# Kernel optimization log

Hardware: AMD Instinct MI355X
Metric: run time of the kernel (lower is better)

## Reference

```python
import jax, jax.numpy as jnp
import numpy as np

B, T, H, NH = 4, 2048, 1024, 16
HD = H // NH  # 64


def setup_inputs() -> dict:
    key = jax.random.key(0)
    ks = jax.random.split(key, 8)
    s = 1.0 / np.sqrt(H)
    return {
        "hidden_states": jax.random.normal(ks[0], (B, T, H), dtype=jnp.float32),
        "attention_mask": jnp.zeros((B, 1, 1, T), dtype=jnp.float32),
        "Wq": jax.random.normal(ks[1], (H, H), dtype=jnp.float32) * s,
        "bq": jax.random.normal(ks[2], (H,), dtype=jnp.float32) * 0.01,
        "Wk": jax.random.normal(ks[3], (H, H), dtype=jnp.float32) * s,
        "bk": jax.random.normal(ks[4], (H,), dtype=jnp.float32) * 0.01,
        "Wv": jax.random.normal(ks[5], (H, H), dtype=jnp.float32) * s,
        "bv": jax.random.normal(ks[6], (H,), dtype=jnp.float32) * 0.01,
    }


def _split_heads(x):
    # [b, t, h*d] -> [b, h, t, d]
    b, t, _ = x.shape
    return x.reshape(b, t, NH, HD).transpose(0, 2, 1, 3)


def reference(hidden_states, attention_mask, Wq, bq, Wk, bk, Wv, bv):
    q = _split_heads(hidden_states @ Wq.T + bq)
    k = _split_heads(hidden_states @ Wk.T + bk)
    v = _split_heads(hidden_states @ Wv.T + bv)
    scores = jnp.einsum('bhqd,bhkd->bhqk', q, k) / jnp.sqrt(jnp.float32(HD))
    t = q.shape[2]
    causal = jnp.triu(jnp.ones((t, t), dtype=scores.dtype), k=1)[None, None] * (-1e9)
    scores = scores + causal + attention_mask
    probs = jax.nn.softmax(scores, axis=-1)
    # module returns [b, h, t, d] (no merge back)
    return jnp.einsum('bhqk,bhkd->bhqd', probs, v)
```

## Files before the change

kernel.cpp:

```cpp
#include <hip/hip_runtime.h>
#include <hip/hip_bf16.h>


typedef float  f32x4 __attribute__((ext_vector_type(4)));
typedef short  s16x8 __attribute__((ext_vector_type(8)));
typedef unsigned short u16;

#define LOG2E 1.44269504088896340736f

__device__ __forceinline__ u16 f2bf(float f) {
  unsigned u = __float_as_uint(f);
  u += 0x7FFFu + ((u >> 16) & 1u);
  return (u16)(u >> 16);
}
__device__ __forceinline__ float bf2f(u16 v) {
  return __uint_as_float(((unsigned)v) << 16);
}
__device__ __forceinline__ float ex2(float x) {
#if __has_builtin(__builtin_amdgcn_exp2f)
  return __builtin_amdgcn_exp2f(x);
#else
  return exp2f(x);
#endif
}
__device__ __forceinline__ float rcp_(float x) {
#if __has_builtin(__builtin_amdgcn_rcpf)
  return __builtin_amdgcn_rcpf(x);
#else
  return 1.0f / x;
#endif
}
__device__ __forceinline__ unsigned cvtpk(float lo, float hi) {
  unsigned r;
  asm("v_cvt_pk_bf16_f32 %0, %1, %2" : "=v"(r) : "v"(lo), "v"(hi));
  return r;
}
__device__ __forceinline__ void bar() {
  asm volatile("" ::: "memory");
  __builtin_amdgcn_s_barrier();
  asm volatile("" ::: "memory");
}

#define GLOAD16(gp, lp)                                                          \
  __builtin_amdgcn_global_load_lds(                                              \
      (const __attribute__((address_space(1))) void*)(gp),                       \
      (__attribute__((address_space(3))) void*)(lp), 16, 0, 0)

#define MFMA(a, b, c) __builtin_amdgcn_mfma_f32_16x16x32_bf16((a), (b), (c), 0, 0, 0)

__global__ __launch_bounds__(256) void cvt_all(
    const float* __restrict__ hs, const float* __restrict__ wq,
    const float* __restrict__ wk, const float* __restrict__ wv,
    const float* __restrict__ maskp,
    u16* __restrict__ xo, u16* __restrict__ qo, u16* __restrict__ ko,
    u16* __restrict__ vo, u16* __restrict__ wm) {
  int b = blockIdx.x;
  const float* s;
  u16* d;
  size_t i;
  bool isw = false;
  if (b < 4096) { s = hs; d = xo; i = (size_t)b * 256 + threadIdx.x; }
  else if (b < 5632) {
    int w = (b - 4096) >> 9, r = (b - 4096) & 511;
    s = (w == 0) ? wq : (w == 1) ? wk : wv;
    d = (w == 0) ? qo : (w == 1) ? ko : vo;
    i = (size_t)r * 256 + threadIdx.x;
  } else {
    s = maskp; d = wm; i = (size_t)(b - 5632) * 256 + threadIdx.x;
    isw = true;
  }
  const float4* sp = (const float4*)s + i * 2;
  float4 a = sp[0], c = sp[1];
  s16x8 r8;
  if (isw) {
    r8[0] = f2bf(ex2(a.x * LOG2E)); r8[1] = f2bf(ex2(a.y * LOG2E));
    r8[2] = f2bf(ex2(a.z * LOG2E)); r8[3] = f2bf(ex2(a.w * LOG2E));
    r8[4] = f2bf(ex2(c.x * LOG2E)); r8[5] = f2bf(ex2(c.y * LOG2E));
    r8[6] = f2bf(ex2(c.z * LOG2E)); r8[7] = f2bf(ex2(c.w * LOG2E));
  } else {
    r8[0] = f2bf(a.x); r8[1] = f2bf(a.y); r8[2] = f2bf(a.z); r8[3] = f2bf(a.w);
    r8[4] = f2bf(c.x); r8[5] = f2bf(c.y); r8[6] = f2bf(c.z); r8[7] = f2bf(c.w);
  }
  *(s16x8*)(d + i * 8) = r8;
}

__global__ __launch_bounds__(512, 2) void qkv_gemm(
    const u16* __restrict__ Xb,
    const u16* __restrict__ Wqb, const u16* __restrict__ Wkb,
    const u16* __restrict__ Wvb,
    const float* __restrict__ bq, const float* __restrict__ bk,
    const float* __restrict__ bv, const u16* __restrict__ Wm,
    u16* __restrict__ Qo, u16* __restrict__ Ko, u16* __restrict__ Vto) {
  int bid0 = blockIdx.x;
  int bid  = (bid0 & 7) * 48 + (bid0 >> 3);
  int which = bid % 3;
  int rt = bid / 3;
  int mt = rt >> 2, nt = rt & 3;
  const u16* W = (which == 0) ? Wqb : (which == 1) ? Wkb : Wvb;
  const float* bias = (which == 0) ? bq : (which == 1) ? bk : bv;

  __shared__ __align__(16) char lds[131072];

  int tid = threadIdx.x;
  int lane = tid & 63, wid = tid >> 6;
  int q16 = lane & 15, g = lane >> 4;
  int wr = wid >> 2, wc = wid & 3;

  int rloc = tid >> 3;
  int sw = ((tid & 7) ^ (rloc & 7)) << 4;
  const char* Asrc = (const char*)Xb + (size_t)(mt * 256 + rloc) * 2048 + sw;
  const char* Bsrc = (const char*)W  + (size_t)(nt * 256 + rloc) * 2048 + sw;

  int slot0 = (g ^ (q16 & 7)) << 4;

#define SA(u, h) do { size_t so = (size_t)(u) * 128 + (size_t)(h) * 262144;      \
    char* dd = lds + ((u) & 1) * 32768 + (h) * 16384 + tid * 16;                 \
    GLOAD16(Asrc + so, dd);                                                      \
    GLOAD16(Asrc + so + 131072, dd + 8192); } while (0)
#define SB(u, h) do { size_t so = (size_t)(u) * 128 + (size_t)(h) * 262144;      \
    char* dd = lds + 65536 + ((u) & 1) * 32768 + (h) * 16384 + tid * 16;         \
    GLOAD16(Bsrc + so, dd);                                                      \
    GLOAD16(Bsrc + so + 131072, dd + 8192); } while (0)

#define LDA8(kh, buf) do {                                                       \
    const char* p_ = lds + (buf) * 32768 + (wr * 128 + q16) * 128 +              \
                     (slot0 ^ ((kh) * 64));                                      \
    _Pragma("unroll")                                                            \
    for (int m_ = 0; m_ < 8; ++m_) fA[m_] = *(const s16x8*)(p_ + m_ * 2048); } while (0)

#define LDB2(nh, kh, buf) do {                                                   \
    const char* p_ = lds + 65536 + (buf) * 32768 +                               \
                     (wc * 64 + (nh) * 32 + q16) * 128 + (slot0 ^ ((kh) * 64));  \
    fB[0] = *(const s16x8*)(p_);                                                 \
    fB[1] = *(const s16x8*)(p_ + 2048); } while (0)

#define MM(nh) do {                                                              \
    __builtin_amdgcn_s_setprio(1);                                               \
    _Pragma("unroll")                                                            \
    for (int m_ = 0; m_ < 8; ++m_) {                                             \
      acc[m_][2 * (nh)]     = MFMA(fA[m_], fB[0], acc[m_][2 * (nh)]);            \
      acc[m_][2 * (nh) + 1] = MFMA(fA[m_], fB[1], acc[m_][2 * (nh) + 1]);        \
    }                                                                            \
    __builtin_amdgcn_s_setprio(0); } while (0)

  SA(0, 0); SA(0, 1); SB(0, 0); SB(0, 1);
  SA(1, 0);
  asm volatile("s_waitcnt vmcnt(2)" ::: "memory");
  bar();

  f32x4 acc[8][4] = {};
  s16x8 fA[8], fB[2];

#pragma unroll 1
  for (int t = 0; t < 16; ++t) {
    int buf = t & 1;
    LDA8(0, buf); LDB2(0, 0, buf);
    if (t < 15) SA(t + 1, 1);
    bar(); MM(0); bar();
    LDB2(1, 0, buf);
    if (t < 15) SB(t + 1, 0);
    bar(); MM(1); bar();
    LDA8(1, buf); LDB2(0, 1, buf);
    if (t < 15) SB(t + 1, 1);
    bar(); MM(0); bar();
    LDB2(1, 1, buf);
    if (t < 14) {
      SA(t + 2, 0);
      asm volatile("s_waitcnt vmcnt(2)" ::: "memory");
    } else if (t == 14) {
      asm volatile("s_waitcnt vmcnt(0)" ::: "memory");
    }
    bar(); MM(1); bar();
  }

  float qsc = (which == 0) ? (0.125f * LOG2E) : 1.0f;
  u16* Out = (which == 0) ? Qo : (which == 1) ? Ko : Vto;
  int h0 = nt * 4 + wc;
  u16* tile = (u16*)(void*)lds + (size_t)wid * 4608;
  const char* tb = (const char*)tile;
  int rl = lane >> 3, cb = (lane & 7) * 16;

#define EPIPASS(P) do {                                                          \
    int mbase = mt * 256 + wr * 128 + (P) * 64;                                  \
    int bb = mbase >> 11, t0 = mbase & 2047;                                     \
    if (which != 2) {                                                            \
      _Pragma("unroll")                                                          \
      for (int n = 0; n < 4; ++n) {                                              \
        float bvl = bias[h0 * 64 + n * 16 + q16];                                \
        _Pragma("unroll")                                                        \
        for (int mm = 0; mm < 4; ++mm)                                           \
          _Pragma("unroll")                                                      \
          for (int j = 0; j < 4; ++j)                                            \
            tile[(mm * 16 + g * 4 + j) * 72 + n * 16 + q16] =                    \
                f2bf((acc[(P) * 4 + mm][n][j] + bvl) * qsc);                     \
      }                                                                          \
    } else {                                                                     \
      const u16* wrow = Wm + (size_t)bb * 2048 + t0;                             \
      float wv[4][4];                                                            \
      _Pragma("unroll")                                                          \
      for (int mm = 0; mm < 4; ++mm)                                             \
        _Pragma("unroll")                                                        \
        for (int j = 0; j < 4; ++j)                                              \
          wv[mm][j] = bf2f(wrow[mm * 16 + g * 4 + j]);                           \
      _Pragma("unroll")                                                          \
      for (int n = 0; n < 4; ++n) {                                              \
        float bvl = bias[h0 * 64 + n * 16 + q16];                                \
        _Pragma("unroll")                                                        \
        for (int mm = 0; mm < 4; ++mm)                                           \
          _Pragma("unroll")                                                      \
          for (int j = 0; j < 4; ++j)                                            \
            tile[(n * 16 + q16) * 72 + mm * 16 + g * 4 + j] =                    \
                f2bf((acc[(P) * 4 + mm][n][j] + bvl) * wv[mm][j]);               \
      }                                                                          \
    }                                                                            \
    asm volatile("" ::: "memory");                                               \
    if (which != 2) {                                                            \
      char* gbase = (char*)(Out + ((size_t)(bb * 16 + h0) * 2048 + t0) * 64);    \
      _Pragma("unroll")                                                          \
      for (int c = 0; c < 8; ++c) {                                              \
        int row = rl + c * 8;                                                    \
        s16x8 v = *(const s16x8*)(tb + row * 144 + cb);                          \
        *(s16x8*)(gbase + row * 128 + cb) = v;                                   \
      }                                                                          \
    } else {                                                                     \
      char* gbase = (char*)Out + ((size_t)(bb * 16 + h0) * 64) * 4096 + t0 * 2;  \
      _Pragma("unroll")                                                          \
      for (int c = 0; c < 8; ++c) {                                              \
        int d = rl + c * 8;                                                      \
        s16x8 v = *(const s16x8*)(tb + d * 144 + cb);                            \
        *(s16x8*)(gbase + (size_t)d * 4096 + cb) = v;                            \
      }                                                                          \
    }                                                                            \
    asm volatile("" ::: "memory"); } while (0)

  EPIPASS(0);
  EPIPASS(1);
#undef EPIPASS
#undef SA
#undef SB
#undef LDA8
#undef LDB2
#undef MM
}

__global__ __launch_bounds__(256, 2) void attn_fwd(
    const u16* __restrict__ Qw, const u16* __restrict__ Kw,
    const u16* __restrict__ Vtw, const u16* __restrict__ Wm,
    float* __restrict__ out) {
  int bid0 = blockIdx.x;
  int bid = (bid0 & 7) * 64 + (bid0 >> 3);
  int bh = bid >> 3, p = bid & 7;
  int tid = threadIdx.x;
  int lane = tid & 63, wid = tid >> 6;
  int q16 = lane & 15, g = lane >> 4;

  __shared__ __align__(16) char Ks[3][8192];
  __shared__ __align__(16) char Vs[3][8192];
  __shared__ __align__(16) u16 wl[2048];

  int srow = tid >> 3;
  int sinner = (tid & 7) << 4;
  int fs = (srow & 7) ^ ((srow >> 1) & 4);
  int ssw = sinner ^ (fs << 4);
  const char* Kg = (const char*)Kw + ((size_t)bh * 2048 + srow) * 128 + ssw;
  const char* Vg = (const char*)Vtw + ((size_t)bh * 64 + srow) * 4096 + ssw;

#define STAGE_T(kt, b) do {                                                      \
    GLOAD16(Kg + (size_t)(kt) * 8192,        Ks[b] + tid * 16);                  \
    GLOAD16(Kg + (size_t)(kt) * 8192 + 4096, Ks[b] + tid * 16 + 4096);           \
    GLOAD16(Vg + (size_t)(kt) * 128,          Vs[b] + tid * 16);                 \
    GLOAD16(Vg + (size_t)(kt) * 128 + 131072, Vs[b] + tid * 16 + 4096); } while (0)

  GLOAD16((const char*)Wm + (size_t)(bh >> 4) * 4096 + tid * 16,
          (char*)wl + tid * 16);

  auto run_phase = [&](int qtl) {
    int nt = 2 * qtl + 2;
    int qw0 = (qtl << 7) + wid * 32;
    size_t qr = (size_t)bh * 2048 + qw0 + q16;
    s16x8 qa[2][2];
#pragma unroll
    for (int h = 0; h < 2; ++h) {
      qa[h][0] = *(const s16x8*)(Qw + (qr + 16 * h) * 64 + g * 8);
      qa[h][1] = *(const s16x8*)(Qw + (qr + 16 * h) * 64 + 32 + g * 8);
    }
    STAGE_T(0, 0);
    STAGE_T(1, 1);

    f32x4 o[2][4] = {};
    f32x4 lw[2] = {};
    int bc = 0;

#pragma unroll 1
    for (int kt = 0; kt < nt; ++kt) {
      if (kt + 2 < nt) {
        int bp = bc + 2; if (bp >= 3) bp -= 3;
        STAGE_T(kt + 2, bp);
        asm volatile("s_waitcnt vmcnt(8)" ::: "memory");
      } else if (kt + 1 < nt) {
        asm volatile("s_waitcnt vmcnt(4)" ::: "memory");
      } else {
        asm volatile("s_waitcnt vmcnt(0)" ::: "memory");
      }
      __builtin_amdgcn_s_barrier();
      asm volatile("" ::: "memory");

      if (64 * kt <= qw0 + 31) {
        int kb = kt << 6;
        const char* ksb = Ks[bc];
        const char* vsb = Vs[bc];
        bool causal = (64 * kt + 63 > qw0);
#pragma unroll
        for (int c = 0; c < 2; ++c) {
          f32x4 sA[2][2];
          __builtin_amdgcn_s_setprio(1);
#pragma unroll
          for (int t4 = 0; t4 < 2; ++t4) {
            int kk = 32 * c + ((q16 >> 2) << 3) + (t4 << 2) + (q16 & 3);
            int fk = (kk & 7) ^ ((kk >> 1) & 4);
            const char* krow = ksb + kk * 128;
            int in0 = (g * 16) ^ (fk << 4);
            s16x8 kf0 = *(const s16x8*)(krow + in0);
            s16x8 kf1 = *(const s16x8*)(krow + (in0 ^ 64));
#pragma unroll
            for (int h = 0; h < 2; ++h) {
              f32x4 sv = {0.f, 0.f, 0.f, 0.f};
              sv = MFMA(kf0, qa[h][0], sv);
              sv = MFMA(kf1, qa[h][1], sv);
              sA[t4][h] = sv;
            }
          }
          __builtin_amdgcn_s_setprio(0);

          s16x8 wf = *(const s16x8*)((const char*)wl + (kb + 32 * c + 8 * g) * 2);

          union { s16x8 v; unsigned u[4]; } pb[2];
#pragma unroll
          for (int h = 0; h < 2; ++h) {
            int qc = qw0 + 16 * h + q16;
#pragma unroll
            for (int t4 = 0; t4 < 2; ++t4) {
              float a0 = ex2(sA[t4][h][0]), a1 = ex2(sA[t4][h][1]);
              float a2 = ex2(sA[t4][h][2]), a3 = ex2(sA[t4][h][3]);
              if (causal) {
                int k0 = kb + 32 * c + 8 * g + 4 * t4;
                a0 = (k0 + 0 <= qc) ? a0 : 0.f;
                a1 = (k0 + 1 <= qc) ? a1 : 0.f;
                a2 = (k0 + 2 <= qc) ? a2 : 0.f;
                a3 = (k0 + 3 <= qc) ? a3 : 0.f;
              }
              pb[h].u[t4 * 2 + 0] = cvtpk(a0, a1);
              pb[h].u[t4 * 2 + 1] = cvtpk(a2, a3);
            }
          }

          __builtin_amdgcn_s_setprio(1);
#pragma unroll
          for (int dt = 0; dt < 4; ++dt) {
            int d = dt * 16 + q16;
            int fv = (d & 7) ^ ((d >> 1) & 4);
            s16x8 vf = *(const s16x8*)(vsb + d * 128 + ((64 * c + 16 * g) ^ (fv << 4)));
#pragma unroll
            for (int h = 0; h < 2; ++h)
              o[h][dt] = MFMA(vf, pb[h].v, o[h][dt]);
          }
#pragma unroll
          for (int h = 0; h < 2; ++h)
            lw[h] = MFMA(wf, pb[h].v, lw[h]);
          __builtin_amdgcn_s_setprio(0);
        }
      }
      __builtin_amdgcn_s_barrier();
      asm volatile("" ::: "memory");
      if (++bc >= 3) bc -= 3;
    }

#pragma unroll
    for (int h = 0; h < 2; ++h) {
      float inv = rcp_(lw[h][0]);
      float* op = out + ((size_t)bh * 2048 + qw0 + 16 * h + q16) * 64 + g * 4;
#pragma unroll
      for (int dt = 0; dt < 4; ++dt)
        *(f32x4*)(op + dt * 16) = o[h][dt] * inv;
    }
  };

  run_phase(15 - p);
  run_phase(p);
#undef STAGE_T
}

extern "C" void kernel_launch(void* const* d_in, const int* in_sizes, int n_in,
                              void* d_out, int out_size, void* d_ws, size_t ws_size,
                              hipStream_t stream) {
  const float* hs   = (const float*)d_in[0];
  const float* mask = (const float*)d_in[1];
  const float* Wq   = (const float*)d_in[2];
  const float* bq   = (const float*)d_in[3];
  const float* Wk   = (const float*)d_in[4];
  const float* bk   = (const float*)d_in[5];
  const float* Wv   = (const float*)d_in[6];
  const float* bv   = (const float*)d_in[7];
  float* out = (float*)d_out;

  char* w = (char*)d_ws;
  u16* Xb  = (u16*)w; w += (size_t)8192 * 1024 * 2;
  u16* Wqb = (u16*)w; w += (size_t)1024 * 1024 * 2;
  u16* Wkb = (u16*)w; w += (size_t)1024 * 1024 * 2;
  u16* Wvb = (u16*)w; w += (size_t)1024 * 1024 * 2;
  u16* Qw  = (u16*)w; w += (size_t)8192 * 1024 * 2;
  u16* Kw  = (u16*)w; w += (size_t)8192 * 1024 * 2;
  u16* Vtw = (u16*)w; w += (size_t)8192 * 1024 * 2;
  u16* Wm  = (u16*)w; w += (size_t)8192 * 2;

  cvt_all<<<5636, 256, 0, stream>>>(hs, Wq, Wk, Wv, mask, Xb, Wqb, Wkb, Wvb, Wm);
  qkv_gemm<<<384, 512, 0, stream>>>(Xb, Wqb, Wkb, Wvb, bq, bk, bv, Wm, Qw, Kw, Vtw);
  attn_fwd<<<512, 256, 0, stream>>>(Qw, Kw, Vtw, Wm, out);
}
```

Baseline: 135.7 us.

## Shrink QKV GEMM tiles to 128x128 with simple double-buffered K loop

Replaces the 256x256, 512-thread QKV projection GEMM that used a 128 KB LDS split-phase pipeline with a 128x128, 256-thread tile that double-buffers 32-wide K slices in 32 KB of LDS. The grid grows from 384 to 1536 blocks with three blocks per CU targeted, trading per-block operand reuse for more parallelism and occupancy across the 256 CUs. The epilogue is reworked for the smaller tile, and the mask weights for V are loaded once outside the passes. The risks are lower arithmetic intensity, more global and LDS traffic per FLOP, and a barrier on every short K step.

After: 136.8 us. Within noise of the previous version (+0.8%).

```diff
diff --git a/kernel.cpp b/kernel.cpp
--- a/kernel.cpp
+++ b/kernel.cpp
@@ -84,7 +84,7 @@
   *(s16x8*)(d + i * 8) = r8;
 }
 
-__global__ __launch_bounds__(512, 2) void qkv_gemm(
+__global__ __launch_bounds__(256, 3) void qkv_gemm(
     const u16* __restrict__ Xb,
     const u16* __restrict__ Wqb, const u16* __restrict__ Wkb,
     const u16* __restrict__ Wvb,
@@ -92,143 +92,126 @@
     const float* __restrict__ bv, const u16* __restrict__ Wm,
     u16* __restrict__ Qo, u16* __restrict__ Ko, u16* __restrict__ Vto) {
   int bid0 = blockIdx.x;
-  int bid  = (bid0 & 7) * 48 + (bid0 >> 3);
+  int bid  = (bid0 & 7) * 192 + (bid0 >> 3);
   int which = bid % 3;
   int rt = bid / 3;
-  int mt = rt >> 2, nt = rt & 3;
+  int mt = rt >> 3, ntl = rt & 7;
   const u16* W = (which == 0) ? Wqb : (which == 1) ? Wkb : Wvb;
   const float* bias = (which == 0) ? bq : (which == 1) ? bk : bv;
 
-  __shared__ __align__(16) char lds[131072];
+  __shared__ __align__(16) char lds[32768];
 
   int tid = threadIdx.x;
   int lane = tid & 63, wid = tid >> 6;
   int q16 = lane & 15, g = lane >> 4;
-  int wr = wid >> 2, wc = wid & 3;
-
-  int rloc = tid >> 3;
-  int sw = ((tid & 7) ^ (rloc & 7)) << 4;
-  const char* Asrc = (const char*)Xb + (size_t)(mt * 256 + rloc) * 2048 + sw;
-  const char* Bsrc = (const char*)W  + (size_t)(nt * 256 + rloc) * 2048 + sw;
-
-  int slot0 = (g ^ (q16 & 7)) << 4;
-
-#define SA(u, h) do { size_t so = (size_t)(u) * 128 + (size_t)(h) * 262144;      \
-    char* dd = lds + ((u) & 1) * 32768 + (h) * 16384 + tid * 16;                 \
-    GLOAD16(Asrc + so, dd);                                                      \
-    GLOAD16(Asrc + so + 131072, dd + 8192); } while (0)
-#define SB(u, h) do { size_t so = (size_t)(u) * 128 + (size_t)(h) * 262144;      \
-    char* dd = lds + 65536 + ((u) & 1) * 32768 + (h) * 16384 + tid * 16;         \
-    GLOAD16(Bsrc + so, dd);                                                      \
-    GLOAD16(Bsrc + so + 131072, dd + 8192); } while (0)
-
-#define LDA8(kh, buf) do {                                                       \
-    const char* p_ = lds + (buf) * 32768 + (wr * 128 + q16) * 128 +              \
-                     (slot0 ^ ((kh) * 64));                                      \
-    _Pragma("unroll")                                                            \
-    for (int m_ = 0; m_ < 8; ++m_) fA[m_] = *(const s16x8*)(p_ + m_ * 2048); } while (0)
-
-#define LDB2(nh, kh, buf) do {                                                   \
-    const char* p_ = lds + 65536 + (buf) * 32768 +                               \
-                     (wc * 64 + (nh) * 32 + q16) * 128 + (slot0 ^ ((kh) * 64));  \
-    fB[0] = *(const s16x8*)(p_);                                                 \
-    fB[1] = *(const s16x8*)(p_ + 2048); } while (0)
-
-#define MM(nh) do {                                                              \
-    __builtin_amdgcn_s_setprio(1);                                               \
-    _Pragma("unroll")                                                            \
-    for (int m_ = 0; m_ < 8; ++m_) {                                             \
-      acc[m_][2 * (nh)]     = MFMA(fA[m_], fB[0], acc[m_][2 * (nh)]);            \
-      acc[m_][2 * (nh) + 1] = MFMA(fA[m_], fB[1], acc[m_][2 * (nh) + 1]);        \
-    }                                                                            \
-    __builtin_amdgcn_s_setprio(0); } while (0)
-
-  SA(0, 0); SA(0, 1); SB(0, 0); SB(0, 1);
-  SA(1, 0);
-  asm volatile("s_waitcnt vmcnt(2)" ::: "memory");
-  bar();
-
-  f32x4 acc[8][4] = {};
-  s16x8 fA[8], fB[2];
+  int wr = wid >> 1, wc = wid & 1;
+
+  int srow = tid >> 2;
+  int ssw = ((tid & 3) ^ (srow & 3)) << 4;
+  const char* Asrc = (const char*)Xb + (size_t)(mt * 128 + srow) * 2048 + ssw;
+  const char* Bsrc = (const char*)W  + (size_t)(ntl * 128 + srow) * 2048 + ssw;
+
+  int slotA = (g ^ (q16 & 3)) << 4;
+
+#define STAGE(i, buf) do { size_t co = (size_t)(i) * 64;                         \
+    GLOAD16(Asrc + co,          lds + (buf) * 8192 + tid * 16);                  \
+    GLOAD16(Asrc + co + 131072, lds + (buf) * 8192 + 4096 + tid * 16);           \
+    GLOAD16(Bsrc + co,          lds + 16384 + (buf) * 8192 + tid * 16);          \
+    GLOAD16(Bsrc + co + 131072, lds + 16384 + (buf) * 8192 + 4096 + tid * 16); } while (0)
+
+  STAGE(0, 0);
+
+  f32x4 acc[4][4] = {};
+  s16x8 af[4], bf[4];
 
 #pragma unroll 1
-  for (int t = 0; t < 16; ++t) {
-    int buf = t & 1;
-    LDA8(0, buf); LDB2(0, 0, buf);
-    if (t < 15) SA(t + 1, 1);
-    bar(); MM(0); bar();
-    LDB2(1, 0, buf);
-    if (t < 15) SB(t + 1, 0);
-    bar(); MM(1); bar();
-    LDA8(1, buf); LDB2(0, 1, buf);
-    if (t < 15) SB(t + 1, 1);
-    bar(); MM(0); bar();
-    LDB2(1, 1, buf);
-    if (t < 14) {
-      SA(t + 2, 0);
-      asm volatile("s_waitcnt vmcnt(2)" ::: "memory");
-    } else if (t == 14) {
+  for (int i = 0; i < 32; ++i) {
+    int buf = i & 1;
+    if (i < 31) {
+      STAGE(i + 1, buf ^ 1);
+      asm volatile("s_waitcnt vmcnt(4)" ::: "memory");
+    } else {
       asm volatile("s_waitcnt vmcnt(0)" ::: "memory");
     }
-    bar(); MM(1); bar();
+    bar();
+    const char* pa = lds + buf * 8192 + (wr * 64 + q16) * 64 + slotA;
+    const char* pb = lds + 16384 + buf * 8192 + (wc * 64 + q16) * 64 + slotA;
+#pragma unroll
+    for (int m = 0; m < 4; ++m) af[m] = *(const s16x8*)(pa + m * 1024);
+#pragma unroll
+    for (int n = 0; n < 4; ++n) bf[n] = *(const s16x8*)(pb + n * 1024);
+    __builtin_amdgcn_s_setprio(1);
+#pragma unroll
+    for (int m = 0; m < 4; ++m)
+#pragma unroll
+      for (int n = 0; n < 4; ++n)
+        acc[m][n] = MFMA(af[m], bf[n], acc[m][n]);
+    __builtin_amdgcn_s_setprio(0);
+    bar();
   }
+#undef STAGE
 
   float qsc = (which == 0) ? (0.125f * LOG2E) : 1.0f;
   u16* Out = (which == 0) ? Qo : (which == 1) ? Ko : Vto;
-  int h0 = nt * 4 + wc;
-  u16* tile = (u16*)(void*)lds + (size_t)wid * 4608;
+  int h0 = ntl * 2 + wc;
+  int m_base = mt * 128 + wr * 64;
+  int bb = m_base >> 11, t0 = m_base & 2047;
+  u16* tile = (u16*)(void*)(lds + wid * 8192);
   const char* tb = (const char*)tile;
   int rl = lane >> 3, cb = (lane & 7) * 16;
 
+  float wv[4][4];
+  if (which == 2) {
+    const u16* wrow = Wm + (size_t)bb * 2048 + t0;
+#pragma unroll
+    for (int m = 0; m < 4; ++m)
+#pragma unroll
+      for (int j = 0; j < 4; ++j)
+        wv[m][j] = bf2f(wrow[m * 16 + g * 4 + j]);
+  }
+
 #define EPIPASS(P) do {                                                          \
-    int mbase = mt * 256 + wr * 128 + (P) * 64;                                  \
-    int bb = mbase >> 11, t0 = mbase & 2047;                                     \
     if (which != 2) {                                                            \
       _Pragma("unroll")                                                          \
-      for (int n = 0; n < 4; ++n) {                                              \
-        float bvl = bias[h0 * 64 + n * 16 + q16];                                \
+      for (int ml = 0; ml < 2; ++ml) {                                           \
         _Pragma("unroll")                                                        \
-        for (int mm = 0; mm < 4; ++mm)                                           \
+        for (int n = 0; n < 4; ++n) {                                            \
+          float bvl = bias[h0 * 64 + n * 16 + q16];                              \
           _Pragma("unroll")                                                      \
           for (int j = 0; j < 4; ++j)                                            \
-            tile[(mm * 16 + g * 4 + j) * 72 + n * 16 + q16] =                    \
-                f2bf((acc[(P) * 4 + mm][n][j] + bvl) * qsc);                     \
+            tile[(ml * 16 + g * 4 + j) * 72 + n * 16 + q16] =                    \
+                f2bf((acc[2 * (P) + ml][n][j] + bvl) * qsc);                     \
+        }                                                                        \
       }                                                                          \
     } else {                                                                     \
-      const u16* wrow = Wm + (size_t)bb * 2048 + t0;                             \
-      float wv[4][4];                                                            \
       _Pragma("unroll")                                                          \
-      for (int mm = 0; mm < 4; ++mm)                                             \
+      for (int nl = 0; nl < 2; ++nl) {                                           \
+        float bvl = bias[h0 * 64 + (2 * (P) + nl) * 16 + q16];                   \
         _Pragma("unroll")                                                        \
-        for (int j = 0; j < 4; ++j)                                              \
-          wv[mm][j] = bf2f(wrow[mm * 16 + g * 4 + j]);                           \
-      _Pragma("unroll")                                                          \
-      for (int n = 0; n < 4; ++n) {                                              \
-        float bvl = bias[h0 * 64 + n * 16 + q16];                                \
-        _Pragma("unroll")                                                        \
-        for (int mm = 0; mm < 4; ++mm)                                           \
+        for (int m = 0; m < 4; ++m)                                              \
           _Pragma("unroll")                                                      \
           for (int j = 0; j < 4; ++j)                                            \
-            tile[(n * 16 + q16) * 72 + mm * 16 + g * 4 + j] =                    \
-                f2bf((acc[(P) * 4 + mm][n][j] + bvl) * wv[mm][j]);               \
+            tile[(nl * 16 + q16) * 72 + m * 16 + g * 4 + j] =                    \
+                f2bf((acc[m][2 * (P) + nl][j] + bvl) * wv[m][j]);                \
       }                                                                          \
     }                                                                            \
     asm volatile("" ::: "memory");                                               \
     if (which != 2) {                                                            \
-      char* gbase = (char*)(Out + ((size_t)(bb * 16 + h0) * 2048 + t0) * 64);    \
+      char* gb = (char*)(Out + ((size_t)(bb * 16 + h0) * 2048 + t0) * 64);       \
       _Pragma("unroll")                                                          \
-      for (int c = 0; c < 8; ++c) {                                              \
+      for (int c = 0; c < 4; ++c) {                                              \
         int row = rl + c * 8;                                                    \
         s16x8 v = *(const s16x8*)(tb + row * 144 + cb);                          \
-        *(s16x8*)(gbase + row * 128 + cb) = v;                                   \
+        *(s16x8*)(gb + (size_t)(32 * (P) + row) * 128 + cb) = v;                 \
       }                                                                          \
     } else {                                                                     \
-      char* gbase = (char*)Out + ((size_t)(bb * 16 + h0) * 64) * 4096 + t0 * 2;  \
+      char* gb = (char*)Out + ((size_t)(bb * 16 + h0) * 64 + 32 * (P)) * 4096 +  \
+                 t0 * 2;                                                         \
       _Pragma("unroll")                                                          \
-      for (int c = 0; c < 8; ++c) {                                              \
-        int d = rl + c * 8;                                                      \
-        s16x8 v = *(const s16x8*)(tb + d * 144 + cb);                            \
-        *(s16x8*)(gbase + (size_t)d * 4096 + cb) = v;                            \
+      for (int c = 0; c < 4; ++c) {                                              \
+        int row = rl + c * 8;                                                    \
+        s16x8 v = *(const s16x8*)(tb + row * 144 + cb);                          \
+        *(s16x8*)(gb + (size_t)row * 4096 + cb) = v;                             \
       }                                                                          \
     }                                                                            \
     asm volatile("" ::: "memory"); } while (0)
@@ -236,11 +219,6 @@
   EPIPASS(0);
   EPIPASS(1);
 #undef EPIPASS
-#undef SA
-#undef SB
-#undef LDA8
-#undef LDB2
-#undef MM
 }
 
 __global__ __launch_bounds__(256, 2) void attn_fwd(
@@ -414,6 +392,6 @@
   u16* Wm  = (u16*)w; w += (size_t)8192 * 2;
 
   cvt_all<<<5636, 256, 0, stream>>>(hs, Wq, Wk, Wv, mask, Xb, Wqb, Wkb, Wvb, Wm);
-  qkv_gemm<<<384, 512, 0, stream>>>(Xb, Wqb, Wkb, Wvb, bq, bk, bv, Wm, Qw, Kw, Vtw);
+  qkv_gemm<<<1536, 256, 0, stream>>>(Xb, Wqb, Wkb, Wvb, bq, bk, bv, Wm, Qw, Kw, Vtw);
   attn_fwd<<<512, 256, 0, stream>>>(Qw, Kw, Vtw, Wm, out);
 }
```

## Retile QKV GEMM to 256x128 blocks and use a 4-buffer attention K/V ring

Applied to the files above, without the earlier changes.

The QKV projection GEMM moves from 512-thread blocks with 256x256 tiles and 128 KB of LDS to 256-thread blocks with 256x128 tiles, a 32-wide k-step, simple double buffering and 48 KB of LDS. This launches twice as many blocks, aiming for better occupancy and fewer barriers per k-step, at the cost of less operand reuse per block. The attention kernel moves from a 3-slot to a 4-slot K/V staging ring and drops the trailing barrier in each iteration, relying on the extra slot to avoid overwriting data other waves are still reading. A barrier is added before staging starts so the second phase cannot overwrite buffers still in use from the first.

Result: faster. 129.5 us, median of 2 (-4.6%).

```diff
diff --git a/kernel.cpp b/kernel.cpp
--- a/kernel.cpp
+++ b/kernel.cpp
@@ -84,7 +84,7 @@
   *(s16x8*)(d + i * 8) = r8;
 }
 
-__global__ __launch_bounds__(512, 2) void qkv_gemm(
+__global__ __launch_bounds__(256, 2) void qkv_gemm(
     const u16* __restrict__ Xb,
     const u16* __restrict__ Wqb, const u16* __restrict__ Wkb,
     const u16* __restrict__ Wvb,
@@ -92,91 +92,71 @@
     const float* __restrict__ bv, const u16* __restrict__ Wm,
     u16* __restrict__ Qo, u16* __restrict__ Ko, u16* __restrict__ Vto) {
   int bid0 = blockIdx.x;
-  int bid  = (bid0 & 7) * 48 + (bid0 >> 3);
+  int bid  = (bid0 & 7) * 96 + (bid0 >> 3);
   int which = bid % 3;
   int rt = bid / 3;
-  int mt = rt >> 2, nt = rt & 3;
+  int mt = rt >> 3, nt = rt & 7;
   const u16* W = (which == 0) ? Wqb : (which == 1) ? Wkb : Wvb;
   const float* bias = (which == 0) ? bq : (which == 1) ? bk : bv;
 
-  __shared__ __align__(16) char lds[131072];
+  __shared__ __align__(16) char lds[49152];
 
   int tid = threadIdx.x;
   int lane = tid & 63, wid = tid >> 6;
   int q16 = lane & 15, g = lane >> 4;
-  int wr = wid >> 2, wc = wid & 3;
-
-  int rloc = tid >> 3;
-  int sw = ((tid & 7) ^ (rloc & 7)) << 4;
-  const char* Asrc = (const char*)Xb + (size_t)(mt * 256 + rloc) * 2048 + sw;
-  const char* Bsrc = (const char*)W  + (size_t)(nt * 256 + rloc) * 2048 + sw;
-
-  int slot0 = (g ^ (q16 & 7)) << 4;
-
-#define SA(u, h) do { size_t so = (size_t)(u) * 128 + (size_t)(h) * 262144;      \
-    char* dd = lds + ((u) & 1) * 32768 + (h) * 16384 + tid * 16;                 \
-    GLOAD16(Asrc + so, dd);                                                      \
-    GLOAD16(Asrc + so + 131072, dd + 8192); } while (0)
-#define SB(u, h) do { size_t so = (size_t)(u) * 128 + (size_t)(h) * 262144;      \
-    char* dd = lds + 65536 + ((u) & 1) * 32768 + (h) * 16384 + tid * 16;         \
-    GLOAD16(Bsrc + so, dd);                                                      \
-    GLOAD16(Bsrc + so + 131072, dd + 8192); } while (0)
-
-#define LDA8(kh, buf) do {                                                       \
-    const char* p_ = lds + (buf) * 32768 + (wr * 128 + q16) * 128 +              \
-                     (slot0 ^ ((kh) * 64));                                      \
-    _Pragma("unroll")                                                            \
-    for (int m_ = 0; m_ < 8; ++m_) fA[m_] = *(const s16x8*)(p_ + m_ * 2048); } while (0)
-
-#define LDB2(nh, kh, buf) do {                                                   \
-    const char* p_ = lds + 65536 + (buf) * 32768 +                               \
-                     (wc * 64 + (nh) * 32 + q16) * 128 + (slot0 ^ ((kh) * 64));  \
-    fB[0] = *(const s16x8*)(p_);                                                 \
-    fB[1] = *(const s16x8*)(p_ + 2048); } while (0)
-
-#define MM(nh) do {                                                              \
-    __builtin_amdgcn_s_setprio(1);                                               \
-    _Pragma("unroll")                                                            \
-    for (int m_ = 0; m_ < 8; ++m_) {                                             \
-      acc[m_][2 * (nh)]     = MFMA(fA[m_], fB[0], acc[m_][2 * (nh)]);            \
-      acc[m_][2 * (nh) + 1] = MFMA(fA[m_], fB[1], acc[m_][2 * (nh) + 1]);        \
-    }                                                                            \
-    __builtin_amdgcn_s_setprio(0); } while (0)
-
-  SA(0, 0); SA(0, 1); SB(0, 0); SB(0, 1);
-  SA(1, 0);
-  asm volatile("s_waitcnt vmcnt(2)" ::: "memory");
-  bar();
+  int wr = wid >> 1, wc = wid & 1;
+
+  int srow = tid >> 2;
+  int sw = (((tid & 3) ^ ((srow >> 1) & 3)) << 4);
+  const char* Asrc = (const char*)Xb + (size_t)(mt * 256 + srow) * 2048 + sw;
+  const char* Bsrc = (const char*)W  + (size_t)(nt * 128 + srow) * 2048 + sw;
+
+  int slotA = (g ^ ((q16 >> 1) & 3)) << 4;
+
+#define STAGE_AB(tt, buf) do { size_t so = (size_t)(tt) * 64;                    \
+    GLOAD16(Asrc + so,          lds + (buf) * 16384 + tid * 16);                 \
+    GLOAD16(Asrc + so + 131072, lds + (buf) * 16384 + 4096 + tid * 16);          \
+    GLOAD16(Asrc + so + 262144, lds + (buf) * 16384 + 8192 + tid * 16);          \
+    GLOAD16(Asrc + so + 393216, lds + (buf) * 16384 + 12288 + tid * 16);         \
+    GLOAD16(Bsrc + so,          lds + 32768 + (buf) * 8192 + tid * 16);          \
+    GLOAD16(Bsrc + so + 131072, lds + 32768 + (buf) * 8192 + 4096 + tid * 16); } while (0)
+
+  STAGE_AB(0, 0);
 
   f32x4 acc[8][4] = {};
-  s16x8 fA[8], fB[2];
+  s16x8 fA[8], fB[4];
 
 #pragma unroll 1
-  for (int t = 0; t < 16; ++t) {
-    int buf = t & 1;
-    LDA8(0, buf); LDB2(0, 0, buf);
-    if (t < 15) SA(t + 1, 1);
-    bar(); MM(0); bar();
-    LDB2(1, 0, buf);
-    if (t < 15) SB(t + 1, 0);
-    bar(); MM(1); bar();
-    LDA8(1, buf); LDB2(0, 1, buf);
-    if (t < 15) SB(t + 1, 1);
-    bar(); MM(0); bar();
-    LDB2(1, 1, buf);
-    if (t < 14) {
-      SA(t + 2, 0);
-      asm volatile("s_waitcnt vmcnt(2)" ::: "memory");
-    } else if (t == 14) {
+  for (int i = 0; i < 32; ++i) {
+    int buf = i & 1;
+    if (i < 31) {
+      STAGE_AB(i + 1, buf ^ 1);
+      asm volatile("s_waitcnt vmcnt(6)" ::: "memory");
+    } else {
       asm volatile("s_waitcnt vmcnt(0)" ::: "memory");
     }
-    bar(); MM(1); bar();
+    bar();
+    const char* pa = lds + buf * 16384 + (wr * 128 + q16) * 64 + slotA;
+    const char* pb = lds + 32768 + buf * 8192 + (wc * 64 + q16) * 64 + slotA;
+#pragma unroll
+    for (int m = 0; m < 8; ++m) fA[m] = *(const s16x8*)(pa + m * 1024);
+#pragma unroll
+    for (int n = 0; n < 4; ++n) fB[n] = *(const s16x8*)(pb + n * 1024);
+    __builtin_amdgcn_s_setprio(1);
+#pragma unroll
+    for (int m = 0; m < 8; ++m)
+#pragma unroll
+      for (int n = 0; n < 4; ++n)
+        acc[m][n] = MFMA(fA[m], fB[n], acc[m][n]);
+    __builtin_amdgcn_s_setprio(0);
+    bar();
   }
+#undef STAGE_AB
 
   float qsc = (which == 0) ? (0.125f * LOG2E) : 1.0f;
   u16* Out = (which == 0) ? Qo : (which == 1) ? Ko : Vto;
-  int h0 = nt * 4 + wc;
-  u16* tile = (u16*)(void*)lds + (size_t)wid * 4608;
+  int h0 = nt * 2 + wc;
+  u16* tile = (u16*)(void*)(lds + wid * 12288);
   const char* tb = (const char*)tile;
   int rl = lane >> 3, cb = (lane & 7) * 16;
 
@@ -236,11 +216,6 @@
   EPIPASS(0);
   EPIPASS(1);
 #undef EPIPASS
-#undef SA
-#undef SB
-#undef LDA8
-#undef LDB2
-#undef MM
 }
 
 __global__ __launch_bounds__(256, 2) void attn_fwd(
@@ -254,8 +229,8 @@
   int lane = tid & 63, wid = tid >> 6;
   int q16 = lane & 15, g = lane >> 4;
 
-  __shared__ __align__(16) char Ks[3][8192];
-  __shared__ __align__(16) char Vs[3][8192];
+  __shared__ __align__(16) char Ks[4][8192];
+  __shared__ __align__(16) char Vs[4][8192];
   __shared__ __align__(16) u16 wl[2048];
 
   int srow = tid >> 3;
@@ -284,31 +259,29 @@
       qa[h][0] = *(const s16x8*)(Qw + (qr + 16 * h) * 64 + g * 8);
       qa[h][1] = *(const s16x8*)(Qw + (qr + 16 * h) * 64 + 32 + g * 8);
     }
+    bar();
     STAGE_T(0, 0);
     STAGE_T(1, 1);
 
     f32x4 o[2][4] = {};
     f32x4 lw[2] = {};
-    int bc = 0;
 
 #pragma unroll 1
     for (int kt = 0; kt < nt; ++kt) {
       if (kt + 2 < nt) {
-        int bp = bc + 2; if (bp >= 3) bp -= 3;
-        STAGE_T(kt + 2, bp);
+        STAGE_T(kt + 2, (kt + 2) & 3);
         asm volatile("s_waitcnt vmcnt(8)" ::: "memory");
       } else if (kt + 1 < nt) {
         asm volatile("s_waitcnt vmcnt(4)" ::: "memory");
       } else {
         asm volatile("s_waitcnt vmcnt(0)" ::: "memory");
       }
-      __builtin_amdgcn_s_barrier();
-      asm volatile("" ::: "memory");
+      bar();
 
       if (64 * kt <= qw0 + 31) {
         int kb = kt << 6;
-        const char* ksb = Ks[bc];
-        const char* vsb = Vs[bc];
+        const char* ksb = Ks[kt & 3];
+        const char* vsb = Vs[kt & 3];
         bool causal = (64 * kt + 63 > qw0);
 #pragma unroll
         for (int c = 0; c < 2; ++c) {
@@ -370,9 +343,6 @@
           __builtin_amdgcn_s_setprio(0);
         }
       }
-      __builtin_amdgcn_s_barrier();
-      asm volatile("" ::: "memory");
-      if (++bc >= 3) bc -= 3;
     }
 
 #pragma unroll
@@ -414,6 +384,6 @@
   u16* Wm  = (u16*)w; w += (size_t)8192 * 2;
 
   cvt_all<<<5636, 256, 0, stream>>>(hs, Wq, Wk, Wv, mask, Xb, Wqb, Wkb, Wvb, Wm);
-  qkv_gemm<<<384, 512, 0, stream>>>(Xb, Wqb, Wkb, Wvb, bq, bk, bv, Wm, Qw, Kw, Vtw);
+  qkv_gemm<<<768, 256, 0, stream>>>(Xb, Wqb, Wkb, Wvb, bq, bk, bv, Wm, Qw, Kw, Vtw);
   attn_fwd<<<512, 256, 0, stream>>>(Qw, Kw, Vtw, Wm, out);
 }
```
